# Optimization experiments

Hardware: AMD Instinct MI355X
Metric: run time of the kernel (lower is better)

## Reference

```python
import jax, jax.numpy as jnp
import numpy as np

D_MODEL = 1024
NUM_HEADS = 16
D_FF = 4096
SEQ = 2048
BATCH = 2
THETA = 10000.0
EPS = 1e-5


def _param(key, shape, fan_in, fan_out):
    std = 2.0 / (fan_in + fan_out) ** 0.5
    return std * jax.random.truncated_normal(key, -3.0, 3.0, shape, dtype=jnp.float32)


def setup_inputs() -> dict:
    key = jax.random.key(0)
    ks = jax.random.split(key, 8)
    d, h, f = D_MODEL, NUM_HEADS, D_FF
    return {
        'x': jax.random.normal(ks[0], (BATCH, SEQ, d), dtype=jnp.float32),
        'token_positions': jnp.arange(SEQ, dtype=jnp.int32),
        'wq': _param(ks[1], (d, d), d, d),
        'wk': _param(ks[2], (d, d), d, d),
        'wv': _param(ks[3], (d, d), d, d),
        'wo': _param(ks[4], (d, d), d, d),
        'ln1_w': jnp.ones((d,), jnp.float32),
        'ln2_w': jnp.ones((d,), jnp.float32),
        'w1': _param(ks[5], (f, d), d, f),
        'w2': _param(ks[6], (d, f), f, d),
        'w3': _param(ks[7], (f, d), d, f),
    }


def rmsnorm(x, w):
    x32 = x.astype(jnp.float32)
    rms = jnp.sqrt(jnp.mean(x32 * x32, axis=-1, keepdims=True) + EPS)
    return ((x32 / rms) * w).astype(x.dtype)


def apply_rope(x, cos, sin):
    # x: [b, h, s, d_k]; cos/sin: [s, d_k//2] -> broadcast as [1,1,s,d_k//2]
    xe, xo = x[..., ::2], x[..., 1::2]
    c = cos[None, None, :, :]
    s = sin[None, None, :, :]
    re = xe * c - xo * s
    ro = xe * s + xo * c
    return jnp.stack((re, ro), axis=-1).reshape(x.shape)


def block_forward(x, token_positions, wq, wk, wv, wo, ln1_w, ln2_w, w1, w2, w3):
    b, s, d = x.shape
    h = NUM_HEADS
    dk = d // h
    # RoPE tables at token positions
    inv_freq = 1.0 / (THETA ** (jnp.arange(0, dk // 2, dtype=jnp.float32) * 2.0 / dk))
    freqs = token_positions.astype(jnp.float32)[:, None] * inv_freq[None, :]  # [s, dk/2]
    cos, sin = jnp.cos(freqs), jnp.sin(freqs)

    # --- attention sublayer (pre-norm) ---
    xn = rmsnorm(x, ln1_w)
    q = jnp.einsum('bsd,ed->bse', xn, wq).reshape(b, s, h, dk).transpose(0, 2, 1, 3)
    k = jnp.einsum('bsd,ed->bse', xn, wk).reshape(b, s, h, dk).transpose(0, 2, 1, 3)
    v = jnp.einsum('bsd,ed->bse', xn, wv).reshape(b, s, h, dk).transpose(0, 2, 1, 3)
    q = apply_rope(q, cos, sin)
    k = apply_rope(k, cos, sin)
    scores = jnp.einsum('bhqd,bhkd->bhqk', q, k) / jnp.sqrt(jnp.float32(dk))
    causal = jnp.tril(jnp.ones((s, s), dtype=bool))
    scores = jnp.where(causal[None, None], scores, -jnp.inf)
    attn = jax.nn.softmax(scores, axis=-1)
    o = jnp.einsum('bhqk,bhkd->bhqd', attn, v)
    o = o.transpose(0, 2, 1, 3).reshape(b, s, d)
    x = x + jnp.einsum('bse,de->bsd', o, wo)

    # --- SwiGLU sublayer (pre-norm) ---
    xn = rmsnorm(x, ln2_w)
    x1 = jnp.einsum('bsd,fd->bsf', xn, w1)
    x3 = jnp.einsum('bsd,fd->bsf', xn, w3)
    gated = (x1 * jax.nn.sigmoid(x1)) * x3
    return x + jnp.einsum('bsf,df->bsd', gated, w2)


def reference(x, token_positions, wq, wk, wv, wo, ln1_w, ln2_w, w1, w2, w3):
    return block_forward(x, token_positions, wq, wk, wv, wo, ln1_w, ln2_w, w1, w2, w3)
```

## Files before the change

kernel.cpp:

```cpp
#include <hip/hip_runtime.h>
#include <hip/hip_bf16.h>

typedef __attribute__((ext_vector_type(4))) float f32x4;
typedef __attribute__((ext_vector_type(8))) short bf16x8;
typedef unsigned short u16;
typedef unsigned int u32;
typedef __attribute__((ext_vector_type(4))) u16 u16x4;

#define DEV static __device__ __forceinline__

constexpr int Bb = 2, Ss = 2048, Dd = 1024, Hh = 16, DKk = 64;
constexpr int Mm = Bb * Ss;

DEV float bf2f(u16 u) { union { u32 i; float f; } v; v.i = (u32)u << 16; return v.f; }
DEV u16 f2bf(float f) {
  union { float f; u32 i; } v; v.f = f;
  u32 r = v.i + 0x7FFFu + ((v.i >> 16) & 1u);
  return (u16)(r >> 16);
}

DEV void gload_lds16(const u16* g, u16* l) {
  __builtin_amdgcn_global_load_lds((const __attribute__((address_space(1))) u32*)g,
                                   (__attribute__((address_space(3))) u32*)l, 16, 0, 0);
}

DEV int swz16(int o) {
  return o ^ (((o >> 8) & 1) << 6) ^ (((o >> 9) & 1) << 5);
}

__global__ void k_cvt_all(const float* __restrict__ wq, const float* __restrict__ wk,
                          const float* __restrict__ wv, const float* __restrict__ wo,
                          const float* __restrict__ w1, const float* __restrict__ w2,
                          const float* __restrict__ w3,
                          u16* __restrict__ wqkv, u16* __restrict__ wob,
                          u16* __restrict__ w13, u16* __restrict__ w2b) {
  int i = (blockIdx.x * 256 + threadIdx.x) * 4;
  int seg = i >> 20;
  const float* src; u16* dst;
  if (seg == 0)      { src = wq + i;             dst = wqkv + i; }
  else if (seg == 1) { src = wk + (i - (1<<20)); dst = wqkv + i; }
  else if (seg == 2) { src = wv + (i - (2<<20)); dst = wqkv + i; }
  else if (seg == 3) { src = wo + (i - (3<<20)); dst = wob  + (i - (3<<20)); }
  else if (seg < 8)  { src = w1 + (i - (4<<20)); dst = w13  + (i - (4<<20)); }
  else if (seg < 12) { src = w2 + (i - (8<<20)); dst = w2b  + (i - (8<<20)); }
  else               { src = w3 + (i - (12<<20)); dst = w13 + (4<<20) + (i - (12<<20)); }
  float4 v = *(const float4*)src;
  u16x4 o = { f2bf(v.x), f2bf(v.y), f2bf(v.z), f2bf(v.w) };
  *(u16x4*)dst = o;
}

__global__ __launch_bounds__(256) void k_rmsnorm(const float* __restrict__ x,
                                                 const float* __restrict__ w,
                                                 u16* __restrict__ out) {
  int row = blockIdx.x;
  int t = threadIdx.x;
  float4 v = ((const float4*)(x + (long)row * Dd))[t];
  float ss = v.x * v.x + v.y * v.y + v.z * v.z + v.w * v.w;
#pragma unroll
  for (int m = 32; m; m >>= 1) ss += __shfl_xor(ss, m, 64);
  __shared__ float red[4];
  if ((t & 63) == 0) red[t >> 6] = ss;
  __syncthreads();
  float tot = red[0] + red[1] + red[2] + red[3];
  float r = rsqrtf(tot * (1.0f / Dd) + 1e-5f);
  float4 wv = ((const float4*)w)[t];
  u16x4 o = { f2bf(v.x * r * wv.x), f2bf(v.y * r * wv.y),
              f2bf(v.z * r * wv.z), f2bf(v.w * r * wv.w) };
  ((u16x4*)(out + (long)row * Dd))[t] = o;
}

__global__ void k_rope(u16* __restrict__ q, u16* __restrict__ k, const int* __restrict__ tp) {
  int idx = blockIdx.x * 256 + threadIdx.x;
  if (idx >= Bb * Ss * Hh * 32) return;
  int p = idx & 31;
  int h = (idx >> 5) & 15;
  int row = idx >> 9;
  int s = row & (Ss - 1);
  float pos = (float)tp[s];
  float invf = __expf(-(float)p * (2.0f / DKk) * 9.2103403719761836f);
  float fr = pos * invf;
  float sn, cs;
  sincosf(fr, &sn, &cs);
  long base = (long)row * Dd + h * DKk + 2 * p;
  float xe = bf2f(q[base]), xo = bf2f(q[base + 1]);
  q[base]     = f2bf((xe * cs - xo * sn) * 0.125f);
  q[base + 1] = f2bf((xe * sn + xo * cs) * 0.125f);
  xe = bf2f(k[base]); xo = bf2f(k[base + 1]);
  k[base]     = f2bf(xe * cs - xo * sn);
  k[base + 1] = f2bf(xe * sn + xo * cs);
}

template <int OM, bool RES>
__global__ __launch_bounds__(256) void k_gemm(const u16* __restrict__ A,
                                              const u16* __restrict__ Bm,
                                              void* __restrict__ Cout,
                                              const float* __restrict__ Rres,
                                              int N, int K) {
  __shared__ u16 Abuf[128 * 32];
  __shared__ u16 Bbuf[128 * 32];
  const int tid = threadIdx.x;
  const int wid = tid >> 6, lane = tid & 63;
  const int wm = wid >> 1, wn = wid & 1;
  const int lq = lane >> 4, ll = lane & 15;
  const int lin = blockIdx.y * gridDim.x + blockIdx.x;
  const int c = lin & 7, j = lin >> 3;
  const int ncc = gridDim.x >> 2;
  const int bxc = (c % ncc) * 4 + (j & 3);
  const int byc = (c / ncc) * 8 + (j >> 2);
  const int m0 = byc * 128, n0 = bxc * 128;

  f32x4 acc[4][4] = {};

  const int srow = tid >> 2;
  const int scol = (tid & 3) * 8;
  const long aoff = (long)(m0 + srow) * K + scol;
  const long boff = (long)(n0 + srow) * K + scol;
  u16* aldsw = Abuf + wid * 512;
  u16* bldsw = Bbuf + wid * 512;

  for (int k0 = 0; k0 < K; k0 += 32) {
    __syncthreads();
    gload_lds16(A + aoff + k0, aldsw);
    gload_lds16(A + aoff + (long)64 * K + k0, aldsw + 2048);
    gload_lds16(Bm + boff + k0, bldsw);
    gload_lds16(Bm + boff + (long)64 * K + k0, bldsw + 2048);
    __syncthreads();
    bf16x8 af[4], bfr[4];
#pragma unroll
    for (int i = 0; i < 4; i++)
      af[i] = *(const bf16x8*)&Abuf[(wm * 64 + i * 16 + ll) * 32 + lq * 8];
#pragma unroll
    for (int j2 = 0; j2 < 4; j2++)
      bfr[j2] = *(const bf16x8*)&Bbuf[(wn * 64 + j2 * 16 + ll) * 32 + lq * 8];
#pragma unroll
    for (int i = 0; i < 4; i++)
#pragma unroll
      for (int j2 = 0; j2 < 4; j2++)
        acc[i][j2] = __builtin_amdgcn_mfma_f32_16x16x32_bf16(af[i], bfr[j2], acc[i][j2], 0, 0, 0);
  }

#pragma unroll
  for (int i = 0; i < 4; i++) {
    const int rowb = m0 + wm * 64 + i * 16 + lq * 4;
#pragma unroll
    for (int j2 = 0; j2 < 4; j2++) {
      const int col = n0 + wn * 64 + j2 * 16 + ll;
#pragma unroll
      for (int r = 0; r < 4; r++) {
        int rr = rowb + r;
        float v = acc[i][j2][r];
        if (RES) v += Rres[(long)rr * N + col];
        if (OM == 1) {
          ((float*)Cout)[(long)rr * N + col] = v;
        } else {
          ((u16*)Cout)[(long)rr * N + col] = f2bf(v);
        }
      }
    }
  }
}

#define STG_A(d, h, kt)                                                         \
  { gload_lds16(A + aoff[0] + (long)(h) * 128 * K + (kt) * 64, &sA[d][h][dst0]); \
    gload_lds16(A + aoff[1] + (long)(h) * 128 * K + (kt) * 64, &sA[d][h][dst1]); }
#define STG_B(d, h, kt)                                                         \
  { gload_lds16(Bp + boff[0] + (long)(h) * 128 * K + (kt) * 64, &sB[d][h][dst0]); \
    gload_lds16(Bp + boff[1] + (long)(h) * 128 * K + (kt) * 64, &sB[d][h][dst1]); }

#define PHASE(q, d, DOB, WVN, ...)                                              \
  {                                                                             \
    bf16x8 af_[2][2];                                                           \
    _Pragma("unroll") for (int s_ = 0; s_ < 2; s_++)                            \
    _Pragma("unroll") for (int kk_ = 0; kk_ < 2; kk_++) {                       \
      int ms_ = (q) * 4 + wm * 2 + s_;                                          \
      int lo_ = ((ms_ & 7) * 16 + ll) * 128 + kk_ * 64 + lq * 16;               \
      af_[s_][kk_] = *(const bf16x8*)((const char*)sA[d][ms_ >> 3] + swz16(lo_)); \
    }                                                                           \
    if (DOB) {                                                                  \
      _Pragma("unroll") for (int ns_ = 0; ns_ < 4; ns_++)                       \
      _Pragma("unroll") for (int kk_ = 0; kk_ < 2; kk_++) {                     \
        int rl_ = wn * 64 + ns_ * 16 + ll;                                      \
        int lo_ = (rl_ & 127) * 128 + kk_ * 64 + lq * 16;                       \
        bfr[ns_][kk_] = *(const bf16x8*)((const char*)sB[d][rl_ >> 7] + swz16(lo_)); \
      }                                                                         \
    }                                                                           \
    __VA_ARGS__;                                                                \
    __builtin_amdgcn_s_barrier();                                               \
    asm volatile("s_waitcnt lgkmcnt(0)" ::: "memory");                          \
    __builtin_amdgcn_sched_barrier(0);                                          \
    __builtin_amdgcn_s_setprio(1);                                              \
    _Pragma("unroll") for (int s_ = 0; s_ < 2; s_++)                            \
    _Pragma("unroll") for (int ns_ = 0; ns_ < 4; ns_++)                         \
    _Pragma("unroll") for (int kk_ = 0; kk_ < 2; kk_++)                         \
      acc[q][s_][ns_] = __builtin_amdgcn_mfma_f32_16x16x32_bf16(                \
          af_[s_][kk_], bfr[ns_][kk_], acc[q][s_][ns_], 0, 0, 0);               \
    __builtin_amdgcn_s_setprio(0);                                              \
    { int wv_ = (WVN);                                                          \
      if (wv_ == 6) { asm volatile("s_waitcnt vmcnt(6)" ::: "memory"); }        \
      else if (wv_ == 0) { asm volatile("s_waitcnt vmcnt(0)" ::: "memory"); } } \
    __builtin_amdgcn_s_barrier();                                               \
  }

template <int OM, int CW, int CH>
__global__ __launch_bounds__(512) void k_gemm8(const u16* __restrict__ A,
                                               const u16* __restrict__ Bm,
                                               void* __restrict__ Cout,
                                               int N, int K) {
  __shared__ u16 sA[2][2][8192];
  __shared__ u16 sB[2][2][8192];
  const int gx = gridDim.x;
  const int lin = blockIdx.y * gx + blockIdx.x;
  const int c = lin & 7, j = lin >> 3;
  const int ncc = gx / CW;
  const int bx = (c % ncc) * CW + j % CW;
  const int by = (c / ncc) * CH + j / CW;
  const long m0 = (long)by * 256, n0 = (long)bx * 256;
  const int tid = threadIdx.x;
  const int wid = tid >> 6, lane = tid & 63;
  const int wm = wid >> 2, wn = wid & 3;
  const int lq = lane >> 4, ll = lane & 15;

  long aoff[2], boff[2];
#pragma unroll
  for (int j2 = 0; j2 < 2; j2++) {
    int off = j2 * 8192 + wid * 1024 + lane * 16;
    int lo = swz16(off);
    int r = lo >> 7, cc = (lo & 127) >> 1;
    aoff[j2] = (m0 + r) * K + cc;
    boff[j2] = (n0 + r) * K + cc;
  }
  const int dst0 = wid * 512;
  const int dst1 = 4096 + wid * 512;

  f32x4 acc[4][2][4];
  bf16x8 bfr[4][2];
  u32 stash[4][2][4][2];

  const int NT = K >> 6;
  const int NI = NT >> 1;
  constexpr int REPS = (OM == 5) ? 2 : 1;

  for (int rep = 0; rep < REPS; rep++) {
    const u16* Bp = Bm + (long)rep * 4096 * K;
    const f32x4 zz = {0.f, 0.f, 0.f, 0.f};
#pragma unroll
    for (int q = 0; q < 4; q++)
#pragma unroll
      for (int s = 0; s < 2; s++)
#pragma unroll
        for (int ns = 0; ns < 4; ns++) acc[q][s][ns] = zz;

    STG_A(0, 0, 0); STG_A(0, 1, 0); STG_B(0, 0, 0); STG_B(0, 1, 0);
    STG_B(1, 0, 1); STG_B(1, 1, 1); STG_A(1, 0, 1);
    asm volatile("s_waitcnt vmcnt(6)" ::: "memory");
    __builtin_amdgcn_s_barrier();

    for (int it = 0; it < NI; it++) {
      const int t = 2 * it;
      const bool full = (t + 2 < NT);
      PHASE(0, 0, true,  -1,            STG_A(1, 1, t + 1))
      PHASE(1, 0, false, -1,            if (full) STG_B(0, 0, t + 2))
      PHASE(2, 0, false, -1,            if (full) STG_B(0, 1, t + 2))
      PHASE(3, 0, false, full ? 6 : 0,  if (full) STG_A(0, 0, t + 2))
      PHASE(0, 1, true,  -1,            if (full) STG_A(0, 1, t + 2))
      PHASE(1, 1, false, -1,            if (full) STG_B(1, 0, t + 3))
      PHASE(2, 1, false, -1,            if (full) STG_B(1, 1, t + 3))
      PHASE(3, 1, false, full ? 6 : -1, if (full) STG_A(1, 0, t + 3))
    }

    if (OM == 5 && rep == 0) {
#pragma unroll
      for (int q = 0; q < 4; q++)
#pragma unroll
        for (int s = 0; s < 2; s++)
#pragma unroll
          for (int ns = 0; ns < 4; ns++) {
            stash[q][s][ns][0] = (u32)f2bf(acc[q][s][ns][0]) | ((u32)f2bf(acc[q][s][ns][1]) << 16);
            stash[q][s][ns][1] = (u32)f2bf(acc[q][s][ns][2]) | ((u32)f2bf(acc[q][s][ns][3]) << 16);
          }
    }
  }

#pragma unroll
  for (int q = 0; q < 4; q++)
#pragma unroll
    for (int s = 0; s < 2; s++) {
      const long row0 = m0 + (q * 4 + wm * 2 + s) * 16 + lq * 4;
#pragma unroll
      for (int ns = 0; ns < 4; ns++) {
        const long col = n0 + wn * 64 + ns * 16 + ll;
#pragma unroll
        for (int r = 0; r < 4; r++) {
          long rr = row0 + r;
          if (OM == 3) {
            float v = acc[q][s][ns][r];
            if (col < 2048) {
              ((u16*)Cout)[(col >> 10) * (long)(Mm * 1024) + rr * 1024 + (col & 1023)] = f2bf(v);
            } else {
              int d = col & 63, hh = ((int)col >> 6) & 15;
              int b2 = (int)rr >> 11, s2 = (int)rr & (Ss - 1);
              ((u16*)Cout)[(long)(2 * Mm * 1024) + ((long)((b2 * Hh + hh) * DKk + d)) * Ss + s2] = f2bf(v);
            }
          } else {
            float v3 = acc[q][s][ns][r];
            u32 st = stash[q][s][ns][r >> 1];
            u16 bb = (r & 1) ? (u16)(st >> 16) : (u16)(st & 0xffffu);
            float v1 = bf2f(bb);
            float g = v1 / (1.0f + __expf(-v1)) * v3;
            ((u16*)Cout)[rr * 4096 + col] = f2bf(g);
          }
        }
      }
    }
}

constexpr int PPAD = 80;

DEV void attn_tile(const u16* __restrict__ Kc, const u16* __restrict__ Vc,
                   u16* __restrict__ myP, const bf16x8* qf, f32x4* accO,
                   float* mrow, float* lrow, int qloc, bool diag, int lq, int ll) {
  f32x4 sacc[4] = {};
#pragma unroll
  for (int fn = 0; fn < 4; fn++)
#pragma unroll
    for (int ks = 0; ks < 2; ks++) {
      bf16x8 kf = *(const bf16x8*)&Kc[(fn * 16 + ll) * 64 + (((ks * 4 + lq) ^ (ll & 7)) * 8)];
      sacc[fn] = __builtin_amdgcn_mfma_f32_16x16x32_bf16(qf[ks], kf, sacc[fn], 0, 0, 0);
    }
  float sv[4][4], pmax[4];
#pragma unroll
  for (int r = 0; r < 4; r++) pmax[r] = -1e30f;
#pragma unroll
  for (int fn = 0; fn < 4; fn++) {
    int kc = fn * 16 + ll;
#pragma unroll
    for (int r = 0; r < 4; r++) {
      float v = sacc[fn][r];
      if (diag && kc > qloc + r) v = -1e30f;
      sv[fn][r] = v;
      pmax[r] = fmaxf(pmax[r], v);
    }
  }
#pragma unroll
  for (int r = 0; r < 4; r++) {
#pragma unroll
    for (int m = 1; m < 16; m <<= 1) pmax[r] = fmaxf(pmax[r], __shfl_xor(pmax[r], m, 64));
  }
  float alpha[4], rsum[4];
#pragma unroll
  for (int r = 0; r < 4; r++) {
    float mnew = fmaxf(mrow[r], pmax[r]);
    alpha[r] = __expf(mrow[r] - mnew);
    mrow[r] = mnew;
    rsum[r] = 0.f;
  }
#pragma unroll
  for (int fn = 0; fn < 4; fn++) {
#pragma unroll
    for (int r = 0; r < 4; r++) {
      float p = __expf(sv[fn][r] - mrow[r]);
      rsum[r] += p;
      myP[(lq * 4 + r) * PPAD + fn * 16 + ll] = f2bf(p);
    }
  }
#pragma unroll
  for (int r = 0; r < 4; r++) {
#pragma unroll
    for (int m = 1; m < 16; m <<= 1) rsum[r] += __shfl_xor(rsum[r], m, 64);
    lrow[r] = lrow[r] * alpha[r] + rsum[r];
  }
#pragma unroll
  for (int fn = 0; fn < 4; fn++)
#pragma unroll
    for (int r = 0; r < 4; r++) accO[fn][r] *= alpha[r];
  bf16x8 pa[2];
#pragma unroll
  for (int ks = 0; ks < 2; ks++)
    pa[ks] = *(const bf16x8*)&myP[ll * PPAD + ks * 32 + lq * 8];
#pragma unroll
  for (int fn = 0; fn < 4; fn++)
#pragma unroll
    for (int ks = 0; ks < 2; ks++) {
      bf16x8 vf = *(const bf16x8*)&Vc[(fn * 16 + ll) * 64 + (((ks * 4 + lq) ^ (ll & 7)) * 8)];
      accO[fn] = __builtin_amdgcn_mfma_f32_16x16x32_bf16(pa[ks], vf, accO[fn], 0, 0, 0);
    }
}

__global__ __launch_bounds__(256) void k_attn(const u16* __restrict__ Q,
                                              const u16* __restrict__ Kb,
                                              const u16* __restrict__ VT,
                                              u16* __restrict__ O) {
  __shared__ u16 Kt[2][64 * 64];
  __shared__ u16 Vt[2][64 * 64];
  __shared__ u16 P[4][16 * PPAD];
  const int pair = blockIdx.x;
  const int bh = blockIdx.y;
  const int b = bh >> 4, h = bh & 15;
  const int tid = threadIdx.x;
  const int wid = tid >> 6, lane = tid & 63;
  const int lq = lane >> 4, ll = lane & 15;
  const int qtA = pair, qtB = 31 - pair;
  const int qr0A = qtA * 64 + wid * 16;
  const int qr0B = qtB * 64 + wid * 16;
  const int qloc = wid * 16 + lq * 4;
  const long qkbase = ((long)b * Ss) * Dd + h * DKk;
  const long vbase  = ((long)(b * Hh + h) * DKk) * Ss;
  const int nk = 32 - pair;

  const int slot0 = wid * 64 + lane;
  const int r0 = slot0 >> 3, c0 = (slot0 & 7) ^ (r0 & 7);
  const int slot1 = 256 + slot0;
  const int r1 = slot1 >> 3, c1 = (slot1 & 7) ^ (r1 & 7);
  const int ldsb0 = (wid * 64) * 8;
  const int ldsb1 = (256 + wid * 64) * 8;

  bf16x8 qfA[2], qfB[2];
#pragma unroll
  for (int ks = 0; ks < 2; ks++) {
    qfA[ks] = *(const bf16x8*)&Q[qkbase + (long)(qr0A + ll) * Dd + ks * 32 + lq * 8];
    qfB[ks] = *(const bf16x8*)&Q[qkbase + (long)(qr0B + ll) * Dd + ks * 32 + lq * 8];
  }

  f32x4 accA[4] = {}, accB[4] = {};
  float mA[4], lA[4], mB[4], lB[4];
#pragma unroll
  for (int r = 0; r < 4; r++) { mA[r] = mB[r] = -1e30f; lA[r] = lB[r] = 0.f; }
  u16* myP = P[wid];

  gload_lds16(Kb + qkbase + (long)r0 * Dd + c0 * 8, Kt[0] + ldsb0);
  gload_lds16(Kb + qkbase + (long)r1 * Dd + c1 * 8, Kt[0] + ldsb1);
  gload_lds16(VT + vbase + (long)r0 * Ss + c0 * 8, Vt[0] + ldsb0);
  gload_lds16(VT + vbase + (long)r1 * Ss + c1 * 8, Vt[0] + ldsb1);
  __syncthreads();

  for (int kt = 0; kt < nk; kt++) {
    if (kt + 1 < nk) {
      const int kn = (kt + 1) * 64;
      u16* kd = Kt[(kt + 1) & 1];
      u16* vd = Vt[(kt + 1) & 1];
      gload_lds16(Kb + qkbase + (long)(kn + r0) * Dd + c0 * 8, kd + ldsb0);
      gload_lds16(Kb + qkbase + (long)(kn + r1) * Dd + c1 * 8, kd + ldsb1);
      gload_lds16(VT + vbase + (long)r0 * Ss + kn + c0 * 8, vd + ldsb0);
      gload_lds16(VT + vbase + (long)r1 * Ss + kn + c1 * 8, vd + ldsb1);
    }
    const u16* Kc = Kt[kt & 1];
    const u16* Vc = Vt[kt & 1];

    attn_tile(Kc, Vc, myP, qfB, accB, mB, lB, qloc, kt == nk - 1, lq, ll);
    if (kt <= pair)
      attn_tile(Kc, Vc, myP, qfA, accA, mA, lA, qloc, kt == pair, lq, ll);
    __syncthreads();
  }

#pragma unroll
  for (int fn = 0; fn < 4; fn++) {
#pragma unroll
    for (int r = 0; r < 4; r++) {
      int rowA = qr0A + lq * 4 + r;
      int rowB = qr0B + lq * 4 + r;
      O[((long)(b * Ss + rowA)) * Dd + h * DKk + fn * 16 + ll] = f2bf(accA[fn][r] / lA[r]);
      O[((long)(b * Ss + rowB)) * Dd + h * DKk + fn * 16 + ll] = f2bf(accB[fn][r] / lB[r]);
    }
  }
}

extern "C" void kernel_launch(void* const* d_in, const int* in_sizes, int n_in,
                              void* d_out, int out_size, void* d_ws, size_t ws_size,
                              hipStream_t stream) {
  const float* x   = (const float*)d_in[0];
  const int*   tp  = (const int*)d_in[1];
  const float* wq  = (const float*)d_in[2];
  const float* wk  = (const float*)d_in[3];
  const float* wv  = (const float*)d_in[4];
  const float* wo  = (const float*)d_in[5];
  const float* ln1 = (const float*)d_in[6];
  const float* ln2 = (const float*)d_in[7];
  const float* w1  = (const float*)d_in[8];
  const float* w2  = (const float*)d_in[9];
  const float* w3  = (const float*)d_in[10];

  char* ws = (char*)d_ws;
  const size_t MB = 1024 * 1024;
  u16*   wqkv_b = (u16*)(ws + 0 * MB);
  u16*   wo_b   = (u16*)(ws + 6 * MB);
  u16*   w13_b  = (u16*)(ws + 8 * MB);
  u16*   w2_b   = (u16*)(ws + 24 * MB);
  u16*   xn     = (u16*)(ws + 32 * MB);
  float* x2     = (float*)(ws + 40 * MB);
  u16*   qb     = (u16*)(ws + 56 * MB);
  u16*   kb     = (u16*)(ws + 64 * MB);
  u16*   vtb    = (u16*)(ws + 72 * MB);
  u16*   ob     = (u16*)(ws + 80 * MB);
  u16*   x1     = (u16*)(ws + 56 * MB);

  k_cvt_all<<<16384, 256, 0, stream>>>(wq, wk, wv, wo, w1, w2, w3,
                                       wqkv_b, wo_b, w13_b, w2_b);
  k_rmsnorm<<<Mm, 256, 0, stream>>>(x, ln1, xn);
  k_gemm8<3, 6, 4><<<dim3(12, 16), 512, 0, stream>>>(xn, wqkv_b, qb, 3072, 1024);
  k_rope<<<(Bb * Ss * Hh * 32) / 256, 256, 0, stream>>>(qb, kb, tp);
  k_attn<<<dim3(16, 32), 256, 0, stream>>>(qb, kb, vtb, ob);
  k_gemm<1, true><<<dim3(8, 32), 256, 0, stream>>>(ob, wo_b, x2, x, 1024, 1024);
  k_rmsnorm<<<Mm, 256, 0, stream>>>(x2, ln2, xn);
  k_gemm8<5, 4, 8><<<dim3(16, 16), 512, 0, stream>>>(xn, w13_b, x1, 4096, 1024);
  k_gemm<1, true><<<dim3(8, 32), 256, 0, stream>>>(x1, w2_b, (float*)d_out, x2, 1024, 4096);
}
```

Baseline: 380.4 us.

## Unfuse SwiGLU gate, split-K the down projection, enlarge attention query tiles

The fused W1/W3 GEMM that stashed the first result in registers is replaced by one wider GEMM that writes x1 and x3 separately, followed by a standalone gating kernel. The down projection is split-K across two z-slices that write fp32 partials, and a separate add kernel sums them with the residual. Attention now processes 32 query rows per wave (128-row tiles paired across the causal triangle) with occupancy hint 2, so each loaded K/V tile serves more queries. These changes remove register pressure from the stash and raise parallelism on the K=4096 GEMM, but add extra global memory traffic and two extra launches.

```diff
diff --git a/kernel.cpp b/kernel.cpp
--- a/kernel.cpp
+++ b/kernel.cpp
@@ -90,12 +90,36 @@
   k[base + 1] = f2bf(xe * sn + xo * cs);
 }
 
+__global__ void k_gate(u16* __restrict__ x1, const u16* __restrict__ x3, int n) {
+  int i = (blockIdx.x * 256 + threadIdx.x) * 4;
+  if (i >= n) return;
+  u16x4 a = *(u16x4*)(x1 + i);
+  u16x4 b = *(const u16x4*)(x3 + i);
+#pragma unroll
+  for (int j = 0; j < 4; j++) {
+    float v = bf2f(a[j]);
+    float g = v / (1.0f + __expf(-v)) * bf2f(b[j]);
+    a[j] = f2bf(g);
+  }
+  *(u16x4*)(x1 + i) = a;
+}
+
+__global__ void k_addout(const float* __restrict__ p0, const float* __restrict__ p1,
+                         const float* __restrict__ x2, float* __restrict__ out) {
+  int i = (blockIdx.x * 256 + threadIdx.x) * 4;
+  float4 a = *(const float4*)(p0 + i);
+  float4 b = *(const float4*)(p1 + i);
+  float4 c = *(const float4*)(x2 + i);
+  float4 o = { a.x + b.x + c.x, a.y + b.y + c.y, a.z + b.z + c.z, a.w + b.w + c.w };
+  *(float4*)(out + i) = o;
+}
+
 template <int OM, bool RES>
 __global__ __launch_bounds__(256) void k_gemm(const u16* __restrict__ A,
                                               const u16* __restrict__ Bm,
                                               void* __restrict__ Cout,
                                               const float* __restrict__ Rres,
-                                              int N, int K) {
+                                              int N, int Kl, int Kstr) {
   __shared__ u16 Abuf[128 * 32];
   __shared__ u16 Bbuf[128 * 32];
   const int tid = threadIdx.x;
@@ -109,21 +133,24 @@
   const int byc = (c / ncc) * 8 + (j >> 2);
   const int m0 = byc * 128, n0 = bxc * 128;
 
+  const u16* Ap = A + (long)blockIdx.z * Kl;
+  const u16* Bp = Bm + (long)blockIdx.z * Kl;
+
   f32x4 acc[4][4] = {};
 
   const int srow = tid >> 2;
   const int scol = (tid & 3) * 8;
-  const long aoff = (long)(m0 + srow) * K + scol;
-  const long boff = (long)(n0 + srow) * K + scol;
+  const long aoff = (long)(m0 + srow) * Kstr + scol;
+  const long boff = (long)(n0 + srow) * Kstr + scol;
   u16* aldsw = Abuf + wid * 512;
   u16* bldsw = Bbuf + wid * 512;
 
-  for (int k0 = 0; k0 < K; k0 += 32) {
+  for (int k0 = 0; k0 < Kl; k0 += 32) {
     __syncthreads();
-    gload_lds16(A + aoff + k0, aldsw);
-    gload_lds16(A + aoff + (long)64 * K + k0, aldsw + 2048);
-    gload_lds16(Bm + boff + k0, bldsw);
-    gload_lds16(Bm + boff + (long)64 * K + k0, bldsw + 2048);
+    gload_lds16(Ap + aoff + k0, aldsw);
+    gload_lds16(Ap + aoff + (long)64 * Kstr + k0, aldsw + 2048);
+    gload_lds16(Bp + boff + k0, bldsw);
+    gload_lds16(Bp + boff + (long)64 * Kstr + k0, bldsw + 2048);
     __syncthreads();
     bf16x8 af[4], bfr[4];
 #pragma unroll
@@ -139,6 +166,7 @@
         acc[i][j2] = __builtin_amdgcn_mfma_f32_16x16x32_bf16(af[i], bfr[j2], acc[i][j2], 0, 0, 0);
   }
 
+  float* fout = (float*)Cout + (long)blockIdx.z * Mm * (long)N;
 #pragma unroll
   for (int i = 0; i < 4; i++) {
     const int rowb = m0 + wm * 64 + i * 16 + lq * 4;
@@ -151,7 +179,7 @@
         float v = acc[i][j2][r];
         if (RES) v += Rres[(long)rr * N + col];
         if (OM == 1) {
-          ((float*)Cout)[(long)rr * N + col] = v;
+          fout[(long)rr * N + col] = v;
         } else {
           ((u16*)Cout)[(long)rr * N + col] = f2bf(v);
         }
@@ -164,8 +192,8 @@
   { gload_lds16(A + aoff[0] + (long)(h) * 128 * K + (kt) * 64, &sA[d][h][dst0]); \
     gload_lds16(A + aoff[1] + (long)(h) * 128 * K + (kt) * 64, &sA[d][h][dst1]); }
 #define STG_B(d, h, kt)                                                         \
-  { gload_lds16(Bp + boff[0] + (long)(h) * 128 * K + (kt) * 64, &sB[d][h][dst0]); \
-    gload_lds16(Bp + boff[1] + (long)(h) * 128 * K + (kt) * 64, &sB[d][h][dst1]); }
+  { gload_lds16(Bm + boff[0] + (long)(h) * 128 * K + (kt) * 64, &sB[d][h][dst0]); \
+    gload_lds16(Bm + boff[1] + (long)(h) * 128 * K + (kt) * 64, &sB[d][h][dst1]); }
 
 #define PHASE(q, d, DOB, WVN, ...)                                              \
   {                                                                             \
@@ -232,53 +260,28 @@
   const int dst0 = wid * 512;
   const int dst1 = 4096 + wid * 512;
 
-  f32x4 acc[4][2][4];
+  f32x4 acc[4][2][4] = {};
   bf16x8 bfr[4][2];
-  u32 stash[4][2][4][2];
 
   const int NT = K >> 6;
   const int NI = NT >> 1;
-  constexpr int REPS = (OM == 5) ? 2 : 1;
-
-  for (int rep = 0; rep < REPS; rep++) {
-    const u16* Bp = Bm + (long)rep * 4096 * K;
-    const f32x4 zz = {0.f, 0.f, 0.f, 0.f};
-#pragma unroll
-    for (int q = 0; q < 4; q++)
-#pragma unroll
-      for (int s = 0; s < 2; s++)
-#pragma unroll
-        for (int ns = 0; ns < 4; ns++) acc[q][s][ns] = zz;
-
-    STG_A(0, 0, 0); STG_A(0, 1, 0); STG_B(0, 0, 0); STG_B(0, 1, 0);
-    STG_B(1, 0, 1); STG_B(1, 1, 1); STG_A(1, 0, 1);
-    asm volatile("s_waitcnt vmcnt(6)" ::: "memory");
-    __builtin_amdgcn_s_barrier();
-
-    for (int it = 0; it < NI; it++) {
-      const int t = 2 * it;
-      const bool full = (t + 2 < NT);
-      PHASE(0, 0, true,  -1,            STG_A(1, 1, t + 1))
-      PHASE(1, 0, false, -1,            if (full) STG_B(0, 0, t + 2))
-      PHASE(2, 0, false, -1,            if (full) STG_B(0, 1, t + 2))
-      PHASE(3, 0, false, full ? 6 : 0,  if (full) STG_A(0, 0, t + 2))
-      PHASE(0, 1, true,  -1,            if (full) STG_A(0, 1, t + 2))
-      PHASE(1, 1, false, -1,            if (full) STG_B(1, 0, t + 3))
-      PHASE(2, 1, false, -1,            if (full) STG_B(1, 1, t + 3))
-      PHASE(3, 1, false, full ? 6 : -1, if (full) STG_A(1, 0, t + 3))
-    }
-
-    if (OM == 5 && rep == 0) {
-#pragma unroll
-      for (int q = 0; q < 4; q++)
-#pragma unroll
-        for (int s = 0; s < 2; s++)
-#pragma unroll
-          for (int ns = 0; ns < 4; ns++) {
-            stash[q][s][ns][0] = (u32)f2bf(acc[q][s][ns][0]) | ((u32)f2bf(acc[q][s][ns][1]) << 16);
-            stash[q][s][ns][1] = (u32)f2bf(acc[q][s][ns][2]) | ((u32)f2bf(acc[q][s][ns][3]) << 16);
-          }
-    }
+
+  STG_A(0, 0, 0); STG_A(0, 1, 0); STG_B(0, 0, 0); STG_B(0, 1, 0);
+  STG_B(1, 0, 1); STG_B(1, 1, 1); STG_A(1, 0, 1);
+  asm volatile("s_waitcnt vmcnt(6)" ::: "memory");
+  __builtin_amdgcn_s_barrier();
+
+  for (int it = 0; it < NI; it++) {
+    const int t = 2 * it;
+    const bool full = (t + 2 < NT);
+    PHASE(0, 0, true,  -1,            STG_A(1, 1, t + 1))
+    PHASE(1, 0, false, -1,            if (full) STG_B(0, 0, t + 2))
+    PHASE(2, 0, false, -1,            if (full) STG_B(0, 1, t + 2))
+    PHASE(3, 0, false, full ? 6 : 0,  if (full) STG_A(0, 0, t + 2))
+    PHASE(0, 1, true,  -1,            if (full) STG_A(0, 1, t + 2))
+    PHASE(1, 1, false, -1,            if (full) STG_B(1, 0, t + 3))
+    PHASE(2, 1, false, -1,            if (full) STG_B(1, 1, t + 3))
+    PHASE(3, 1, false, full ? 6 : -1, if (full) STG_A(1, 0, t + 3))
   }
 
 #pragma unroll
@@ -291,9 +294,9 @@
         const long col = n0 + wn * 64 + ns * 16 + ll;
 #pragma unroll
         for (int r = 0; r < 4; r++) {
+          float v = acc[q][s][ns][r];
           long rr = row0 + r;
           if (OM == 3) {
-            float v = acc[q][s][ns][r];
             if (col < 2048) {
               ((u16*)Cout)[(col >> 10) * (long)(Mm * 1024) + rr * 1024 + (col & 1023)] = f2bf(v);
             } else {
@@ -302,12 +305,7 @@
               ((u16*)Cout)[(long)(2 * Mm * 1024) + ((long)((b2 * Hh + hh) * DKk + d)) * Ss + s2] = f2bf(v);
             }
           } else {
-            float v3 = acc[q][s][ns][r];
-            u32 st = stash[q][s][ns][r >> 1];
-            u16 bb = (r & 1) ? (u16)(st >> 16) : (u16)(st & 0xffffu);
-            float v1 = bf2f(bb);
-            float g = v1 / (1.0f + __expf(-v1)) * v3;
-            ((u16*)Cout)[rr * 4096 + col] = f2bf(g);
+            ((u16*)Cout)[(col >> 12) * ((long)Mm * 4096) + rr * 4096 + (col & 4095)] = f2bf(v);
           }
         }
       }
@@ -316,96 +314,106 @@
 
 constexpr int PPAD = 80;
 
-DEV void attn_tile(const u16* __restrict__ Kc, const u16* __restrict__ Vc,
-                   u16* __restrict__ myP, const bf16x8* qf, f32x4* accO,
-                   float* mrow, float* lrow, int qloc, bool diag, int lq, int ll) {
-  f32x4 sacc[4] = {};
+DEV void attn_tile2(const u16* __restrict__ Kc, const u16* __restrict__ Vc,
+                    u16* __restrict__ myP, const bf16x8 (*qf)[2], f32x4 (*accO)[4],
+                    float* mrow, float* lrow,
+                    int qbase, bool domask, int kbase, int lq, int ll) {
+  f32x4 sacc[2][4] = {};
 #pragma unroll
   for (int fn = 0; fn < 4; fn++)
 #pragma unroll
     for (int ks = 0; ks < 2; ks++) {
       bf16x8 kf = *(const bf16x8*)&Kc[(fn * 16 + ll) * 64 + (((ks * 4 + lq) ^ (ll & 7)) * 8)];
-      sacc[fn] = __builtin_amdgcn_mfma_f32_16x16x32_bf16(qf[ks], kf, sacc[fn], 0, 0, 0);
-    }
-  float sv[4][4], pmax[4];
-#pragma unroll
-  for (int r = 0; r < 4; r++) pmax[r] = -1e30f;
-#pragma unroll
-  for (int fn = 0; fn < 4; fn++) {
-    int kc = fn * 16 + ll;
+#pragma unroll
+      for (int g = 0; g < 2; g++)
+        sacc[g][fn] = __builtin_amdgcn_mfma_f32_16x16x32_bf16(qf[g][ks], kf, sacc[g][fn], 0, 0, 0);
+    }
+#pragma unroll
+  for (int g = 0; g < 2; g++) {
+    float pmax[4];
+#pragma unroll
+    for (int r = 0; r < 4; r++) pmax[r] = -1e30f;
+#pragma unroll
+    for (int fn = 0; fn < 4; fn++) {
+      int kc = kbase + fn * 16 + ll;
+#pragma unroll
+      for (int r = 0; r < 4; r++) {
+        float v = sacc[g][fn][r];
+        if (domask && kc > qbase + g * 16 + lq * 4 + r) v = -1e30f;
+        sacc[g][fn][r] = v;
+        pmax[r] = fmaxf(pmax[r], v);
+      }
+    }
 #pragma unroll
     for (int r = 0; r < 4; r++) {
-      float v = sacc[fn][r];
-      if (diag && kc > qloc + r) v = -1e30f;
-      sv[fn][r] = v;
-      pmax[r] = fmaxf(pmax[r], v);
-    }
-  }
-#pragma unroll
-  for (int r = 0; r < 4; r++) {
-#pragma unroll
-    for (int m = 1; m < 16; m <<= 1) pmax[r] = fmaxf(pmax[r], __shfl_xor(pmax[r], m, 64));
-  }
-  float alpha[4], rsum[4];
-#pragma unroll
-  for (int r = 0; r < 4; r++) {
-    float mnew = fmaxf(mrow[r], pmax[r]);
-    alpha[r] = __expf(mrow[r] - mnew);
-    mrow[r] = mnew;
-    rsum[r] = 0.f;
-  }
-#pragma unroll
-  for (int fn = 0; fn < 4; fn++) {
+#pragma unroll
+      for (int m = 1; m < 16; m <<= 1) pmax[r] = fmaxf(pmax[r], __shfl_xor(pmax[r], m, 64));
+    }
+    float alpha[4], rsum[4];
 #pragma unroll
     for (int r = 0; r < 4; r++) {
-      float p = __expf(sv[fn][r] - mrow[r]);
-      rsum[r] += p;
-      myP[(lq * 4 + r) * PPAD + fn * 16 + ll] = f2bf(p);
-    }
-  }
-#pragma unroll
-  for (int r = 0; r < 4; r++) {
-#pragma unroll
-    for (int m = 1; m < 16; m <<= 1) rsum[r] += __shfl_xor(rsum[r], m, 64);
-    lrow[r] = lrow[r] * alpha[r] + rsum[r];
-  }
-#pragma unroll
-  for (int fn = 0; fn < 4; fn++)
-#pragma unroll
-    for (int r = 0; r < 4; r++) accO[fn][r] *= alpha[r];
-  bf16x8 pa[2];
-#pragma unroll
-  for (int ks = 0; ks < 2; ks++)
-    pa[ks] = *(const bf16x8*)&myP[ll * PPAD + ks * 32 + lq * 8];
+      float mnew = fmaxf(mrow[g * 4 + r], pmax[r]);
+      alpha[r] = __expf(mrow[g * 4 + r] - mnew);
+      mrow[g * 4 + r] = mnew;
+      rsum[r] = 0.f;
+    }
+#pragma unroll
+    for (int fn = 0; fn < 4; fn++) {
+#pragma unroll
+      for (int r = 0; r < 4; r++) {
+        float p = __expf(sacc[g][fn][r] - mrow[g * 4 + r]);
+        rsum[r] += p;
+        myP[(g * 16 + lq * 4 + r) * PPAD + fn * 16 + ll] = f2bf(p);
+      }
+    }
+#pragma unroll
+    for (int r = 0; r < 4; r++) {
+#pragma unroll
+      for (int m = 1; m < 16; m <<= 1) rsum[r] += __shfl_xor(rsum[r], m, 64);
+      lrow[g * 4 + r] = lrow[g * 4 + r] * alpha[r] + rsum[r];
+    }
+#pragma unroll
+    for (int fn = 0; fn < 4; fn++)
+#pragma unroll
+      for (int r = 0; r < 4; r++) accO[g][fn][r] *= alpha[r];
+  }
+  bf16x8 pa[2][2];
+#pragma unroll
+  for (int g = 0; g < 2; g++)
+#pragma unroll
+    for (int ks = 0; ks < 2; ks++)
+      pa[g][ks] = *(const bf16x8*)&myP[(g * 16 + ll) * PPAD + ks * 32 + lq * 8];
 #pragma unroll
   for (int fn = 0; fn < 4; fn++)
 #pragma unroll
     for (int ks = 0; ks < 2; ks++) {
       bf16x8 vf = *(const bf16x8*)&Vc[(fn * 16 + ll) * 64 + (((ks * 4 + lq) ^ (ll & 7)) * 8)];
-      accO[fn] = __builtin_amdgcn_mfma_f32_16x16x32_bf16(pa[ks], vf, accO[fn], 0, 0, 0);
-    }
-}
-
-__global__ __launch_bounds__(256) void k_attn(const u16* __restrict__ Q,
-                                              const u16* __restrict__ Kb,
-                                              const u16* __restrict__ VT,
-                                              u16* __restrict__ O) {
+#pragma unroll
+      for (int g = 0; g < 2; g++)
+        accO[g][fn] = __builtin_amdgcn_mfma_f32_16x16x32_bf16(pa[g][ks], vf, accO[g][fn], 0, 0, 0);
+    }
+}
+
+__global__ __launch_bounds__(256, 2) void k_attn(const u16* __restrict__ Q,
+                                                 const u16* __restrict__ Kb,
+                                                 const u16* __restrict__ VT,
+                                                 u16* __restrict__ O) {
   __shared__ u16 Kt[2][64 * 64];
   __shared__ u16 Vt[2][64 * 64];
-  __shared__ u16 P[4][16 * PPAD];
+  __shared__ u16 P[4][32 * PPAD];
   const int pair = blockIdx.x;
   const int bh = blockIdx.y;
   const int b = bh >> 4, h = bh & 15;
   const int tid = threadIdx.x;
   const int wid = tid >> 6, lane = tid & 63;
   const int lq = lane >> 4, ll = lane & 15;
-  const int qtA = pair, qtB = 31 - pair;
-  const int qr0A = qtA * 64 + wid * 16;
-  const int qr0B = qtB * 64 + wid * 16;
-  const int qloc = wid * 16 + lq * 4;
+  const int qtA = pair, qtB = 15 - pair;
+  const int qr0A = qtA * 128 + wid * 32;
+  const int qr0B = qtB * 128 + wid * 32;
   const long qkbase = ((long)b * Ss) * Dd + h * DKk;
   const long vbase  = ((long)(b * Hh + h) * DKk) * Ss;
-  const int nk = 32 - pair;
+  const int nkA = 2 * qtA + 2;
+  const int nkB = 2 * qtB + 2;
 
   const int slot0 = wid * 64 + lane;
   const int r0 = slot0 >> 3, c0 = (slot0 & 7) ^ (r0 & 7);
@@ -414,17 +422,19 @@
   const int ldsb0 = (wid * 64) * 8;
   const int ldsb1 = (256 + wid * 64) * 8;
 
-  bf16x8 qfA[2], qfB[2];
-#pragma unroll
-  for (int ks = 0; ks < 2; ks++) {
-    qfA[ks] = *(const bf16x8*)&Q[qkbase + (long)(qr0A + ll) * Dd + ks * 32 + lq * 8];
-    qfB[ks] = *(const bf16x8*)&Q[qkbase + (long)(qr0B + ll) * Dd + ks * 32 + lq * 8];
-  }
-
-  f32x4 accA[4] = {}, accB[4] = {};
-  float mA[4], lA[4], mB[4], lB[4];
-#pragma unroll
-  for (int r = 0; r < 4; r++) { mA[r] = mB[r] = -1e30f; lA[r] = lB[r] = 0.f; }
+  bf16x8 qfA[2][2], qfB[2][2];
+#pragma unroll
+  for (int g = 0; g < 2; g++)
+#pragma unroll
+    for (int ks = 0; ks < 2; ks++) {
+      qfA[g][ks] = *(const bf16x8*)&Q[qkbase + (long)(qr0A + g * 16 + ll) * Dd + ks * 32 + lq * 8];
+      qfB[g][ks] = *(const bf16x8*)&Q[qkbase + (long)(qr0B + g * 16 + ll) * Dd + ks * 32 + lq * 8];
+    }
+
+  f32x4 accA[2][4] = {}, accB[2][4] = {};
+  float mA[8], lA[8], mB[8], lB[8];
+#pragma unroll
+  for (int r = 0; r < 8; r++) { mA[r] = mB[r] = -1e30f; lA[r] = lB[r] = 0.f; }
   u16* myP = P[wid];
 
   gload_lds16(Kb + qkbase + (long)r0 * Dd + c0 * 8, Kt[0] + ldsb0);
@@ -433,8 +443,8 @@
   gload_lds16(VT + vbase + (long)r1 * Ss + c1 * 8, Vt[0] + ldsb1);
   __syncthreads();
 
-  for (int kt = 0; kt < nk; kt++) {
-    if (kt + 1 < nk) {
+  for (int kt = 0; kt < nkB; kt++) {
+    if (kt + 1 < nkB) {
       const int kn = (kt + 1) * 64;
       u16* kd = Kt[(kt + 1) & 1];
       u16* vd = Vt[(kt + 1) & 1];
@@ -446,22 +456,26 @@
     const u16* Kc = Kt[kt & 1];
     const u16* Vc = Vt[kt & 1];
 
-    attn_tile(Kc, Vc, myP, qfB, accB, mB, lB, qloc, kt == nk - 1, lq, ll);
-    if (kt <= pair)
-      attn_tile(Kc, Vc, myP, qfA, accA, mA, lA, qloc, kt == pair, lq, ll);
+    attn_tile2(Kc, Vc, myP, qfB, accB, mB, lB, wid * 32,
+               kt >= nkB - 2, (kt - (nkB - 2)) * 64, lq, ll);
+    if (kt < nkA)
+      attn_tile2(Kc, Vc, myP, qfA, accA, mA, lA, wid * 32,
+                 kt >= nkA - 2, (kt - (nkA - 2)) * 64, lq, ll);
     __syncthreads();
   }
 
 #pragma unroll
-  for (int fn = 0; fn < 4; fn++) {
-#pragma unroll
-    for (int r = 0; r < 4; r++) {
-      int rowA = qr0A + lq * 4 + r;
-      int rowB = qr0B + lq * 4 + r;
-      O[((long)(b * Ss + rowA)) * Dd + h * DKk + fn * 16 + ll] = f2bf(accA[fn][r] / lA[r]);
-      O[((long)(b * Ss + rowB)) * Dd + h * DKk + fn * 16 + ll] = f2bf(accB[fn][r] / lB[r]);
-    }
-  }
+  for (int g = 0; g < 2; g++)
+#pragma unroll
+    for (int fn = 0; fn < 4; fn++) {
+#pragma unroll
+      for (int r = 0; r < 4; r++) {
+        int rowA = qr0A + g * 16 + lq * 4 + r;
+        int rowB = qr0B + g * 16 + lq * 4 + r;
+        O[((long)(b * Ss + rowA)) * Dd + h * DKk + fn * 16 + ll] = f2bf(accA[g][fn][r] / lA[g * 4 + r]);
+        O[((long)(b * Ss + rowB)) * Dd + h * DKk + fn * 16 + ll] = f2bf(accB[g][fn][r] / lB[g * 4 + r]);
+      }
+    }
 }
 
 extern "C" void kernel_launch(void* const* d_in, const int* in_sizes, int n_in,
@@ -492,15 +506,20 @@
   u16*   vtb    = (u16*)(ws + 72 * MB);
   u16*   ob     = (u16*)(ws + 80 * MB);
   u16*   x1     = (u16*)(ws + 56 * MB);
+  u16*   x3     = (u16*)(ws + 88 * MB);
+  float* p0     = (float*)(ws + 88 * MB);
+  float* p1     = (float*)(ws + 104 * MB);
 
   k_cvt_all<<<16384, 256, 0, stream>>>(wq, wk, wv, wo, w1, w2, w3,
                                        wqkv_b, wo_b, w13_b, w2_b);
   k_rmsnorm<<<Mm, 256, 0, stream>>>(x, ln1, xn);
   k_gemm8<3, 6, 4><<<dim3(12, 16), 512, 0, stream>>>(xn, wqkv_b, qb, 3072, 1024);
   k_rope<<<(Bb * Ss * Hh * 32) / 256, 256, 0, stream>>>(qb, kb, tp);
-  k_attn<<<dim3(16, 32), 256, 0, stream>>>(qb, kb, vtb, ob);
-  k_gemm<1, true><<<dim3(8, 32), 256, 0, stream>>>(ob, wo_b, x2, x, 1024, 1024);
+  k_attn<<<dim3(8, 32), 256, 0, stream>>>(qb, kb, vtb, ob);
+  k_gemm<1, true><<<dim3(8, 32), 256, 0, stream>>>(ob, wo_b, x2, x, 1024, 1024, 1024);
   k_rmsnorm<<<Mm, 256, 0, stream>>>(x2, ln2, xn);
-  k_gemm8<5, 4, 8><<<dim3(16, 16), 512, 0, stream>>>(xn, w13_b, x1, 4096, 1024);
-  k_gemm<1, true><<<dim3(8, 32), 256, 0, stream>>>(x1, w2_b, (float*)d_out, x2, 1024, 4096);
-}
+  k_gemm8<4, 4, 8><<<dim3(32, 16), 512, 0, stream>>>(xn, w13_b, x1, 8192, 1024);
+  k_gate<<<16384, 256, 0, stream>>>(x1, x3, 4096 * 4096);
+  k_gemm<1, false><<<dim3(8, 32, 2), 256, 0, stream>>>(x1, w2_b, p0, nullptr, 1024, 2048, 4096);
+  k_addout<<<4096, 256, 0, stream>>>(p0, p1, x2, (float*)d_out);
+}
```

Result: slower. 408.9 us (+7.5%).
